# Kernel tuning notes

Measured on AMD Instinct MI355X. Metric: run time of the kernel, lower is better.

Reference implementation:

```python
import jax, jax.numpy as jnp
import numpy as np

WIDTH = 2048
NUM_HEADS = 16
HEAD_DIM = WIDTH // NUM_HEADS
BATCH = 16384


def block_diag_linear(x, w, b):
    # x: [..., width] -> [..., h, i] einsum with w: [h, i, j]
    xh = x.reshape(x.shape[:-1] + (NUM_HEADS, HEAD_DIM))
    y = jnp.einsum('...hi,hij->...hj', xh, w) + b
    return y.reshape(x.shape)


def setup_inputs() -> dict:
    key = jax.random.key(0)
    ks = jax.random.split(key, 7)
    x = jax.random.normal(ks[0], (BATCH, WIDTH), dtype=jnp.float32)
    state = jax.random.normal(ks[1], (BATCH, WIDTH), dtype=jnp.float32)
    w_in = jax.random.normal(ks[2], (NUM_HEADS, HEAD_DIM, HEAD_DIM), dtype=jnp.float32) * 0.02
    b_in = jax.random.normal(ks[3], (NUM_HEADS, HEAD_DIM), dtype=jnp.float32) * 0.02
    w_a = jax.random.normal(ks[4], (NUM_HEADS, HEAD_DIM, HEAD_DIM), dtype=jnp.float32) * 0.02
    b_a = jax.random.normal(ks[5], (NUM_HEADS, HEAD_DIM), dtype=jnp.float32) * 0.02
    a_param = jax.random.normal(ks[6], (WIDTH,), dtype=jnp.float32) * 0.5
    return {'x': x, 'state': state, 'w_in': w_in, 'b_in': b_in,
            'w_a': w_a, 'b_a': b_a, 'a_param': a_param}


def reference(x, state, w_in, b_in, w_a, b_a, a_param):
    gate_x = jax.nn.sigmoid(block_diag_linear(x, w_in, b_in))
    gate_a = jax.nn.sigmoid(block_diag_linear(x, w_a, b_a))
    log_a = -8.0 * gate_a * jax.nn.softplus(a_param)  # [B, width]
    a = jnp.exp(log_a)
    scale = jnp.sqrt(1.0 - jnp.exp(2.0 * log_a))
    return a * state + gate_x * x * scale
```

## Files before the change

### kernel.cpp

```cpp
#include <hip/hip_runtime.h>
#include <hip/hip_bf16.h>

typedef __attribute__((ext_vector_type(8))) short bf16x8;
typedef __attribute__((ext_vector_type(4))) float f32x4;
typedef __attribute__((ext_vector_type(4))) unsigned short u16x4;
typedef __attribute__((ext_vector_type(8))) unsigned short u16x8;

#define WIDTH  2048
#define NHEADS 16
#define HDIM   128
#define BM     64

__device__ __forceinline__ unsigned short f2bf(float f) {
  union { float f; unsigned int u; } v; v.f = f;
  unsigned int u = v.u;
  unsigned int r = (u + 0x7FFFu + ((u >> 16) & 1u)) >> 16;
  return (unsigned short)r;
}

__device__ __forceinline__ float bf2f(unsigned short s) {
  union { unsigned int u; float f; } v;
  v.u = ((unsigned int)s) << 16;
  return v.f;
}

__device__ __forceinline__ unsigned int pk_bf16(float lo, float hi) {
  __hip_bfloat162 b = __float22bfloat162_rn(make_float2(lo, hi));
  union { __hip_bfloat162 b; unsigned int u; } c; c.b = b;
  return c.u;
}

#define LOG2E 1.4426950408889634f

__global__ __launch_bounds__(256) void prep_kernel(
    const float* __restrict__ w_in, const float* __restrict__ w_a,
    const float* __restrict__ a_param,
    const float* __restrict__ b_in, const float* __restrict__ b_a,
    unsigned short* __restrict__ wTin, unsigned short* __restrict__ wTa,
    float* __restrict__ sp8, float* __restrict__ sbi, float* __restrict__ sba) {
  const int b = blockIdx.x;
  if (b >= 64) {
    int tid = (b - 64) * 256 + threadIdx.x;
    float v  = a_param[tid];
    float sp = (v > 20.0f) ? v : log1pf(__expf(v));
    sp8[tid] = 8.0f * sp * LOG2E;
    sbi[tid] = b_in[tid] * LOG2E;
    sba[tid] = b_a[tid] * LOG2E;
    return;
  }
  const int h  = b >> 2;
  const int i0 = (b & 3) * 32;
  __shared__ unsigned short tl[2][32][136];

  const float* s0 = w_in + h * 16384 + i0 * 128;
  const float* s1 = w_a  + h * 16384 + i0 * 128;
#pragma unroll
  for (int it = 0; it < 4; ++it) {
    int e = it * 1024 + threadIdx.x * 4;
    int r = e >> 7, c = e & 127;
    f32x4 v0 = *reinterpret_cast<const f32x4*>(s0 + r * 128 + c);
    f32x4 v1 = *reinterpret_cast<const f32x4*>(s1 + r * 128 + c);
#pragma unroll
    for (int k = 0; k < 4; ++k) {
      tl[0][r][c + k] = f2bf(v0[k] * LOG2E);
      tl[1][r][c + k] = f2bf(v1[k] * LOG2E);
    }
  }
  __syncthreads();

  const int j  = threadIdx.x >> 1;
  const int ih = (threadIdx.x & 1) * 16;
  u16x8 o0a, o0b, o1a, o1b;
#pragma unroll
  for (int k = 0; k < 8; ++k) {
    o0a[k] = tl[0][ih + k][j];      o0b[k] = tl[0][ih + 8 + k][j];
    o1a[k] = tl[1][ih + k][j];      o1b[k] = tl[1][ih + 8 + k][j];
  }
  unsigned short* d0 = wTin + h * 16384 + j * 128 + i0 + ih;
  unsigned short* d1 = wTa  + h * 16384 + j * 128 + i0 + ih;
  *reinterpret_cast<u16x8*>(d0)     = o0a;
  *reinterpret_cast<u16x8*>(d0 + 8) = o0b;
  *reinterpret_cast<u16x8*>(d1)     = o1a;
  *reinterpret_cast<u16x8*>(d1 + 8) = o1b;
}

__global__ __launch_bounds__(256, 4) void rglru_kernel(
    const float* __restrict__ x, const float* __restrict__ state,
    const float* __restrict__ sbi, const float* __restrict__ sba,
    const unsigned short* __restrict__ wTin, const unsigned short* __restrict__ wTa,
    const float* __restrict__ sp8, float* __restrict__ out) {
  __shared__ unsigned short xs[BM * HDIM];

  const int bid  = blockIdx.x;
  const int h    = bid & (NHEADS - 1);
  const int rb   = bid >> 4;
  const int t    = threadIdx.x;
  const int lane = t & 63;
  const int wid  = t >> 6;
  const int l15  = lane & 15;
  const int l4   = lane >> 4;

  const float* xtile = x + (long)rb * BM * WIDTH + h * HDIM;
#pragma unroll
  for (int it = 0; it < 8; ++it) {
    int idx = it * 256 + t;
    int r   = idx >> 5;
    int c4  = idx & 31;
    f32x4 v = __builtin_nontemporal_load(
        reinterpret_cast<const f32x4*>(xtile + (long)r * WIDTH) + c4);
    uint2 p;
    p.x = pk_bf16(v[0], v[1]);
    p.y = pk_bf16(v[2], v[3]);
    int off = (r * 256 + c4 * 8) ^ ((r & 7) << 4);
    *reinterpret_cast<uint2*>(reinterpret_cast<char*>(xs) + off) = p;
  }

  const int cb = h * HDIM + wid * 32 + l4 * 4;
  f32x4 bi0 = *reinterpret_cast<const f32x4*>(sbi + cb);
  f32x4 bi1 = *reinterpret_cast<const f32x4*>(sbi + cb + 16);
  f32x4 ba0 = *reinterpret_cast<const f32x4*>(sba + cb);
  f32x4 ba1 = *reinterpret_cast<const f32x4*>(sba + cb + 16);
  f32x4 sp0 = *reinterpret_cast<const f32x4*>(sp8 + cb);
  f32x4 sp1 = *reinterpret_cast<const f32x4*>(sp8 + cb + 16);

  __syncthreads();

  f32x4 acc_in[4][2], acc_a[4][2];
#pragma unroll
  for (int m = 0; m < 4; ++m) {
    acc_in[m][0] = bi0; acc_in[m][1] = bi1;
    acc_a[m][0]  = ba0; acc_a[m][1]  = ba1;
  }

  const unsigned short* wi0 = wTin + ((h * HDIM + wid * 32 + l15) * HDIM) + l4 * 8;
  const unsigned short* wi1 = wi0 + 16 * HDIM;
  const unsigned short* wa0 = wTa + ((h * HDIM + wid * 32 + l15) * HDIM) + l4 * 8;
  const unsigned short* wa1 = wa0 + 16 * HDIM;

  const int xsw = ((l15 & 7) << 4);

#pragma unroll
  for (int kk = 0; kk < 4; ++kk) {
    bf16x8 xfr[4];
#pragma unroll
    for (int m = 0; m < 4; ++m) {
      int boff = ((m * 16 + l15) * 256 + kk * 64 + l4 * 16) ^ xsw;
      xfr[m] = *reinterpret_cast<const bf16x8*>(
          reinterpret_cast<const char*>(xs) + boff);
    }
    bf16x8 win[2], wa[2];
    win[0] = *reinterpret_cast<const bf16x8*>(wi0 + kk * 32);
    win[1] = *reinterpret_cast<const bf16x8*>(wi1 + kk * 32);
    wa[0]  = *reinterpret_cast<const bf16x8*>(wa0 + kk * 32);
    wa[1]  = *reinterpret_cast<const bf16x8*>(wa1 + kk * 32);
#pragma unroll
    for (int m = 0; m < 4; ++m)
#pragma unroll
      for (int n = 0; n < 2; ++n) {
        acc_in[m][n] = __builtin_amdgcn_mfma_f32_16x16x32_bf16(
            win[n], xfr[m], acc_in[m][n], 0, 0, 0);
        acc_a[m][n] = __builtin_amdgcn_mfma_f32_16x16x32_bf16(
            wa[n], xfr[m], acc_a[m][n], 0, 0, 0);
      }
  }

  const long base = (long)(rb * BM + l15) * WIDTH + cb;
  const float* ps = state + base;
  float*       po = out + base;
  const char* pxs = reinterpret_cast<const char*>(xs);
  const int xe0 = (l15 * 256 + (wid * 32 + l4 * 4) * 2) ^ xsw;
  const int xe1 = (l15 * 256 + (wid * 32 + 16 + l4 * 4) * 2) ^ xsw;

#pragma unroll
  for (int m = 0; m < 4; ++m) {
#pragma unroll
    for (int n = 0; n < 2; ++n) {
      f32x4 sv = *reinterpret_cast<const f32x4*>(ps + n * 16);
      u16x4 xb = *reinterpret_cast<const u16x4*>(
          pxs + (n ? xe1 : xe0) + m * 4096);
      f32x4 sp = n ? sp1 : sp0;
      f32x4 o;
#pragma unroll
      for (int r = 0; r < 4; ++r) {
        float gx  = __builtin_amdgcn_rcpf(1.0f + exp2f(-acc_in[m][n][r]));
        float ga  = __builtin_amdgcn_rcpf(1.0f + exp2f(-acc_a[m][n][r]));
        float av  = exp2f(-ga * sp[r]);
        float sc  = sqrtf(fmaxf(1.0f - av * av, 0.0f));
        o[r] = av * sv[r] + gx * bf2f(xb[r]) * sc;
      }
      *reinterpret_cast<f32x4*>(po + n * 16) = o;
    }
    ps += 16 * WIDTH;
    po += 16 * WIDTH;
  }
}

extern "C" void kernel_launch(void* const* d_in, const int* in_sizes, int n_in,
                              void* d_out, int out_size, void* d_ws, size_t ws_size,
                              hipStream_t stream) {
  const float* x       = (const float*)d_in[0];
  const float* state   = (const float*)d_in[1];
  const float* w_in    = (const float*)d_in[2];
  const float* b_in    = (const float*)d_in[3];
  const float* w_a     = (const float*)d_in[4];
  const float* b_a     = (const float*)d_in[5];
  const float* a_param = (const float*)d_in[6];
  float* out = (float*)d_out;

  unsigned short* wTin = (unsigned short*)d_ws;
  unsigned short* wTa  = wTin + NHEADS * HDIM * HDIM;
  float*          sp8  = (float*)(wTa + NHEADS * HDIM * HDIM);
  float*          sbi  = sp8 + WIDTH;
  float*          sba  = sbi + WIDTH;

  hipLaunchKernelGGL(prep_kernel, dim3(72), dim3(256), 0, stream,
                     w_in, w_a, a_param, b_in, b_a, wTin, wTa, sp8, sbi, sba);

  hipLaunchKernelGGL(rglru_kernel, dim3(4096), dim3(256), 0, stream,
                     x, state, sbi, sba, wTin, wTa, sp8, out);
}
```

Baseline: 103.4 us.

## Drop shared-memory x staging; load x fragments directly and transpose via identity MFMA

Each wave now owns 16 rows and all 128 output columns of a head. It loads its x fragments straight from global memory into registers, which removes the LDS tile and the __syncthreads. In the epilogue, x values in the output layout come from an MFMA against an identity matrix instead of LDS reads. Each wave must now stream the full per-head weight matrix (8 column tiles) from global/L2, which raises weight load traffic and register pressure. The x loads are no longer nontemporal and read only 32-byte chunks per lane.

```diff
diff --git a/kernel.cpp b/kernel.cpp
--- a/kernel.cpp
+++ b/kernel.cpp
@@ -3,25 +3,17 @@
 
 typedef __attribute__((ext_vector_type(8))) short bf16x8;
 typedef __attribute__((ext_vector_type(4))) float f32x4;
-typedef __attribute__((ext_vector_type(4))) unsigned short u16x4;
 typedef __attribute__((ext_vector_type(8))) unsigned short u16x8;
 
 #define WIDTH  2048
 #define NHEADS 16
 #define HDIM   128
-#define BM     64
 
 __device__ __forceinline__ unsigned short f2bf(float f) {
   union { float f; unsigned int u; } v; v.f = f;
   unsigned int u = v.u;
   unsigned int r = (u + 0x7FFFu + ((u >> 16) & 1u)) >> 16;
   return (unsigned short)r;
-}
-
-__device__ __forceinline__ float bf2f(unsigned short s) {
-  union { unsigned int u; float f; } v;
-  v.u = ((unsigned int)s) << 16;
-  return v.f;
 }
 
 __device__ __forceinline__ unsigned int pk_bf16(float lo, float hi) {
@@ -89,8 +81,6 @@
     const float* __restrict__ sbi, const float* __restrict__ sba,
     const unsigned short* __restrict__ wTin, const unsigned short* __restrict__ wTa,
     const float* __restrict__ sp8, float* __restrict__ out) {
-  __shared__ unsigned short xs[BM * HDIM];
-
   const int bid  = blockIdx.x;
   const int h    = bid & (NHEADS - 1);
   const int rb   = bid >> 4;
@@ -100,98 +90,84 @@
   const int l15  = lane & 15;
   const int l4   = lane >> 4;
 
-  const float* xtile = x + (long)rb * BM * WIDTH + h * HDIM;
+  const int  r0   = rb * 64 + wid * 16;
+  const long rowo = (long)(r0 + l15) * WIDTH + h * HDIM;
+
+  const float* xrow = x + rowo + l4 * 8;
+  f32x4 xq[4][2];
 #pragma unroll
-  for (int it = 0; it < 8; ++it) {
-    int idx = it * 256 + t;
-    int r   = idx >> 5;
-    int c4  = idx & 31;
-    f32x4 v = __builtin_nontemporal_load(
-        reinterpret_cast<const f32x4*>(xtile + (long)r * WIDTH) + c4);
-    uint2 p;
-    p.x = pk_bf16(v[0], v[1]);
-    p.y = pk_bf16(v[2], v[3]);
-    int off = (r * 256 + c4 * 8) ^ ((r & 7) << 4);
-    *reinterpret_cast<uint2*>(reinterpret_cast<char*>(xs) + off) = p;
+  for (int kk = 0; kk < 4; ++kk) {
+    xq[kk][0] = *reinterpret_cast<const f32x4*>(xrow + kk * 32);
+    xq[kk][1] = *reinterpret_cast<const f32x4*>(xrow + kk * 32 + 4);
+  }
+  bf16x8 xfr[4];
+#pragma unroll
+  for (int kk = 0; kk < 4; ++kk) {
+    union { bf16x8 v; unsigned int u[4]; } uu;
+    uu.u[0] = pk_bf16(xq[kk][0][0], xq[kk][0][1]);
+    uu.u[1] = pk_bf16(xq[kk][0][2], xq[kk][0][3]);
+    uu.u[2] = pk_bf16(xq[kk][1][0], xq[kk][1][1]);
+    uu.u[3] = pk_bf16(xq[kk][1][2], xq[kk][1][3]);
+    xfr[kk] = uu.v;
   }
 
-  const int cb = h * HDIM + wid * 32 + l4 * 4;
-  f32x4 bi0 = *reinterpret_cast<const f32x4*>(sbi + cb);
-  f32x4 bi1 = *reinterpret_cast<const f32x4*>(sbi + cb + 16);
-  f32x4 ba0 = *reinterpret_cast<const f32x4*>(sba + cb);
-  f32x4 ba1 = *reinterpret_cast<const f32x4*>(sba + cb + 16);
-  f32x4 sp0 = *reinterpret_cast<const f32x4*>(sp8 + cb);
-  f32x4 sp1 = *reinterpret_cast<const f32x4*>(sp8 + cb + 16);
-
-  __syncthreads();
-
-  f32x4 acc_in[4][2], acc_a[4][2];
+  bf16x8 idf0, idf1;
+  {
+    union { bf16x8 v; unsigned short us[8]; } a0, a1;
 #pragma unroll
-  for (int m = 0; m < 4; ++m) {
-    acc_in[m][0] = bi0; acc_in[m][1] = bi1;
-    acc_a[m][0]  = ba0; acc_a[m][1]  = ba1;
+    for (int e = 0; e < 8; ++e) {
+      int k = l4 * 8 + e;
+      a0.us[e] = (k == l15)      ? (unsigned short)0x3F80 : (unsigned short)0;
+      a1.us[e] = (k == l15 + 16) ? (unsigned short)0x3F80 : (unsigned short)0;
+    }
+    idf0 = a0.v; idf1 = a1.v;
   }
 
-  const unsigned short* wi0 = wTin + ((h * HDIM + wid * 32 + l15) * HDIM) + l4 * 8;
-  const unsigned short* wi1 = wi0 + 16 * HDIM;
-  const unsigned short* wa0 = wTa + ((h * HDIM + wid * 32 + l15) * HDIM) + l4 * 8;
-  const unsigned short* wa1 = wa0 + 16 * HDIM;
+  const int cbase = h * HDIM + l4 * 4;
+  f32x4 acc_in[8], acc_a[8];
+#pragma unroll
+  for (int n = 0; n < 8; ++n) {
+    acc_in[n] = *reinterpret_cast<const f32x4*>(sbi + cbase + n * 16);
+    acc_a[n]  = *reinterpret_cast<const f32x4*>(sba + cbase + n * 16);
+  }
 
-  const int xsw = ((l15 & 7) << 4);
+  const unsigned short* wb0 = wTin + (h * HDIM + l15) * HDIM + l4 * 8;
+  const unsigned short* wb1 = wTa  + (h * HDIM + l15) * HDIM + l4 * 8;
 
 #pragma unroll
   for (int kk = 0; kk < 4; ++kk) {
-    bf16x8 xfr[4];
+    const unsigned short* w0 = wb0 + kk * 32;
+    const unsigned short* w1 = wb1 + kk * 32;
 #pragma unroll
-    for (int m = 0; m < 4; ++m) {
-      int boff = ((m * 16 + l15) * 256 + kk * 64 + l4 * 16) ^ xsw;
-      xfr[m] = *reinterpret_cast<const bf16x8*>(
-          reinterpret_cast<const char*>(xs) + boff);
+    for (int n = 0; n < 8; ++n) {
+      bf16x8 wi = *reinterpret_cast<const bf16x8*>(w0 + n * 16 * HDIM);
+      bf16x8 wv = *reinterpret_cast<const bf16x8*>(w1 + n * 16 * HDIM);
+      acc_in[n] = __builtin_amdgcn_mfma_f32_16x16x32_bf16(wi, xfr[kk], acc_in[n], 0, 0, 0);
+      acc_a[n]  = __builtin_amdgcn_mfma_f32_16x16x32_bf16(wv, xfr[kk], acc_a[n], 0, 0, 0);
     }
-    bf16x8 win[2], wa[2];
-    win[0] = *reinterpret_cast<const bf16x8*>(wi0 + kk * 32);
-    win[1] = *reinterpret_cast<const bf16x8*>(wi1 + kk * 32);
-    wa[0]  = *reinterpret_cast<const bf16x8*>(wa0 + kk * 32);
-    wa[1]  = *reinterpret_cast<const bf16x8*>(wa1 + kk * 32);
-#pragma unroll
-    for (int m = 0; m < 4; ++m)
-#pragma unroll
-      for (int n = 0; n < 2; ++n) {
-        acc_in[m][n] = __builtin_amdgcn_mfma_f32_16x16x32_bf16(
-            win[n], xfr[m], acc_in[m][n], 0, 0, 0);
-        acc_a[m][n] = __builtin_amdgcn_mfma_f32_16x16x32_bf16(
-            wa[n], xfr[m], acc_a[m][n], 0, 0, 0);
-      }
   }
 
-  const long base = (long)(rb * BM + l15) * WIDTH + cb;
-  const float* ps = state + base;
-  float*       po = out + base;
-  const char* pxs = reinterpret_cast<const char*>(xs);
-  const int xe0 = (l15 * 256 + (wid * 32 + l4 * 4) * 2) ^ xsw;
-  const int xe1 = (l15 * 256 + (wid * 32 + 16 + l4 * 4) * 2) ^ xsw;
+  const float* srow = state + rowo + l4 * 4;
+  float*       orow = out + rowo + l4 * 4;
+  const float* spb  = sp8 + cbase;
+  const f32x4  zero = (f32x4)(0.0f);
 
 #pragma unroll
-  for (int m = 0; m < 4; ++m) {
+  for (int n = 0; n < 8; ++n) {
+    f32x4 sv = *reinterpret_cast<const f32x4*>(srow + n * 16);
+    f32x4 sp = *reinterpret_cast<const f32x4*>(spb + n * 16);
+    f32x4 xt = __builtin_amdgcn_mfma_f32_16x16x32_bf16(
+        (n & 1) ? idf1 : idf0, xfr[n >> 1], zero, 0, 0, 0);
+    f32x4 o;
 #pragma unroll
-    for (int n = 0; n < 2; ++n) {
-      f32x4 sv = *reinterpret_cast<const f32x4*>(ps + n * 16);
-      u16x4 xb = *reinterpret_cast<const u16x4*>(
-          pxs + (n ? xe1 : xe0) + m * 4096);
-      f32x4 sp = n ? sp1 : sp0;
-      f32x4 o;
-#pragma unroll
-      for (int r = 0; r < 4; ++r) {
-        float gx  = __builtin_amdgcn_rcpf(1.0f + exp2f(-acc_in[m][n][r]));
-        float ga  = __builtin_amdgcn_rcpf(1.0f + exp2f(-acc_a[m][n][r]));
-        float av  = exp2f(-ga * sp[r]);
-        float sc  = sqrtf(fmaxf(1.0f - av * av, 0.0f));
-        o[r] = av * sv[r] + gx * bf2f(xb[r]) * sc;
-      }
-      *reinterpret_cast<f32x4*>(po + n * 16) = o;
+    for (int r = 0; r < 4; ++r) {
+      float gx = __builtin_amdgcn_rcpf(1.0f + exp2f(-acc_in[n][r]));
+      float ga = __builtin_amdgcn_rcpf(1.0f + exp2f(-acc_a[n][r]));
+      float av = exp2f(-ga * sp[r]);
+      float sc = sqrtf(fmaxf(1.0f - av * av, 0.0f));
+      o[r] = av * sv[r] + gx * xt[r] * sc;
     }
-    ps += 16 * WIDTH;
-    po += 16 * WIDTH;
+    *reinterpret_cast<f32x4*>(orow + n * 16) = o;
   }
 }
 
```

Result: slower. 224.2 us (+116.9%).

## Process two row tiles per block, prefetching second x tile during first compute

Applied to the files above, without the earlier changes.

Each block now handles two 64-row tiles instead of one, halving the grid. The second tile's x values are loaded into registers before the first tile's MFMA and epilogue run, then converted and written to a second LDS buffer. This overlaps global load latency with compute and amortises weight and bias loads across two tiles. In exchange it uses more registers and LDS per block, which may reduce occupancy, and leaves fewer blocks to balance across CUs.

```diff
diff --git a/kernel.cpp b/kernel.cpp
--- a/kernel.cpp
+++ b/kernel.cpp
@@ -89,30 +89,32 @@
     const float* __restrict__ sbi, const float* __restrict__ sba,
     const unsigned short* __restrict__ wTin, const unsigned short* __restrict__ wTa,
     const float* __restrict__ sp8, float* __restrict__ out) {
-  __shared__ unsigned short xs[BM * HDIM];
+  __shared__ unsigned short xs[2][BM * HDIM];
 
   const int bid  = blockIdx.x;
   const int h    = bid & (NHEADS - 1);
-  const int rb   = bid >> 4;
+  const int rbb  = bid >> 4;
   const int t    = threadIdx.x;
   const int lane = t & 63;
   const int wid  = t >> 6;
   const int l15  = lane & 15;
   const int l4   = lane >> 4;
 
-  const float* xtile = x + (long)rb * BM * WIDTH + h * HDIM;
+  const int r_  = t >> 5;
+  const int c4_ = t & 31;
+
+  const float* xt0 = x + (long)(rbb * 2 * BM) * WIDTH + h * HDIM;
+
 #pragma unroll
   for (int it = 0; it < 8; ++it) {
-    int idx = it * 256 + t;
-    int r   = idx >> 5;
-    int c4  = idx & 31;
+    int r = it * 8 + r_;
     f32x4 v = __builtin_nontemporal_load(
-        reinterpret_cast<const f32x4*>(xtile + (long)r * WIDTH) + c4);
+        reinterpret_cast<const f32x4*>(xt0 + (long)r * WIDTH) + c4_);
     uint2 p;
     p.x = pk_bf16(v[0], v[1]);
     p.y = pk_bf16(v[2], v[3]);
-    int off = (r * 256 + c4 * 8) ^ ((r & 7) << 4);
-    *reinterpret_cast<uint2*>(reinterpret_cast<char*>(xs) + off) = p;
+    int off = (r * 256 + c4_ * 8) ^ ((r & 7) << 4);
+    *reinterpret_cast<uint2*>(reinterpret_cast<char*>(xs[0]) + off) = p;
   }
 
   const int cb = h * HDIM + wid * 32 + l4 * 4;
@@ -123,75 +125,102 @@
   f32x4 sp0 = *reinterpret_cast<const f32x4*>(sp8 + cb);
   f32x4 sp1 = *reinterpret_cast<const f32x4*>(sp8 + cb + 16);
 
-  __syncthreads();
-
-  f32x4 acc_in[4][2], acc_a[4][2];
-#pragma unroll
-  for (int m = 0; m < 4; ++m) {
-    acc_in[m][0] = bi0; acc_in[m][1] = bi1;
-    acc_a[m][0]  = ba0; acc_a[m][1]  = ba1;
-  }
-
   const unsigned short* wi0 = wTin + ((h * HDIM + wid * 32 + l15) * HDIM) + l4 * 8;
   const unsigned short* wi1 = wi0 + 16 * HDIM;
   const unsigned short* wa0 = wTa + ((h * HDIM + wid * 32 + l15) * HDIM) + l4 * 8;
   const unsigned short* wa1 = wa0 + 16 * HDIM;
 
   const int xsw = ((l15 & 7) << 4);
-
-#pragma unroll
-  for (int kk = 0; kk < 4; ++kk) {
-    bf16x8 xfr[4];
-#pragma unroll
-    for (int m = 0; m < 4; ++m) {
-      int boff = ((m * 16 + l15) * 256 + kk * 64 + l4 * 16) ^ xsw;
-      xfr[m] = *reinterpret_cast<const bf16x8*>(
-          reinterpret_cast<const char*>(xs) + boff);
-    }
-    bf16x8 win[2], wa[2];
-    win[0] = *reinterpret_cast<const bf16x8*>(wi0 + kk * 32);
-    win[1] = *reinterpret_cast<const bf16x8*>(wi1 + kk * 32);
-    wa[0]  = *reinterpret_cast<const bf16x8*>(wa0 + kk * 32);
-    wa[1]  = *reinterpret_cast<const bf16x8*>(wa1 + kk * 32);
-#pragma unroll
-    for (int m = 0; m < 4; ++m)
-#pragma unroll
-      for (int n = 0; n < 2; ++n) {
-        acc_in[m][n] = __builtin_amdgcn_mfma_f32_16x16x32_bf16(
-            win[n], xfr[m], acc_in[m][n], 0, 0, 0);
-        acc_a[m][n] = __builtin_amdgcn_mfma_f32_16x16x32_bf16(
-            wa[n], xfr[m], acc_a[m][n], 0, 0, 0);
-      }
-  }
-
-  const long base = (long)(rb * BM + l15) * WIDTH + cb;
-  const float* ps = state + base;
-  float*       po = out + base;
-  const char* pxs = reinterpret_cast<const char*>(xs);
   const int xe0 = (l15 * 256 + (wid * 32 + l4 * 4) * 2) ^ xsw;
   const int xe1 = (l15 * 256 + (wid * 32 + 16 + l4 * 4) * 2) ^ xsw;
 
-#pragma unroll
-  for (int m = 0; m < 4; ++m) {
-#pragma unroll
-    for (int n = 0; n < 2; ++n) {
-      f32x4 sv = *reinterpret_cast<const f32x4*>(ps + n * 16);
-      u16x4 xb = *reinterpret_cast<const u16x4*>(
-          pxs + (n ? xe1 : xe0) + m * 4096);
-      f32x4 sp = n ? sp1 : sp0;
-      f32x4 o;
-#pragma unroll
-      for (int r = 0; r < 4; ++r) {
-        float gx  = __builtin_amdgcn_rcpf(1.0f + exp2f(-acc_in[m][n][r]));
-        float ga  = __builtin_amdgcn_rcpf(1.0f + exp2f(-acc_a[m][n][r]));
-        float av  = exp2f(-ga * sp[r]);
-        float sc  = sqrtf(fmaxf(1.0f - av * av, 0.0f));
-        o[r] = av * sv[r] + gx * bf2f(xb[r]) * sc;
+  __syncthreads();
+
+  f32x4 xa[8];
+  {
+    const float* xt1 = xt0 + (long)BM * WIDTH;
+#pragma unroll
+    for (int it = 0; it < 8; ++it) {
+      int r = it * 8 + r_;
+      xa[it] = __builtin_nontemporal_load(
+          reinterpret_cast<const f32x4*>(xt1 + (long)r * WIDTH) + c4_);
+    }
+  }
+
+#pragma unroll
+  for (int tile = 0; tile < 2; ++tile) {
+    f32x4 acc_in[4][2], acc_a[4][2];
+#pragma unroll
+    for (int m = 0; m < 4; ++m) {
+      acc_in[m][0] = bi0; acc_in[m][1] = bi1;
+      acc_a[m][0]  = ba0; acc_a[m][1]  = ba1;
+    }
+
+    const char* pxs = reinterpret_cast<const char*>(xs[tile]);
+
+#pragma unroll
+    for (int kk = 0; kk < 4; ++kk) {
+      bf16x8 xfr[4];
+#pragma unroll
+      for (int m = 0; m < 4; ++m) {
+        int boff = ((m * 16 + l15) * 256 + kk * 64 + l4 * 16) ^ xsw;
+        xfr[m] = *reinterpret_cast<const bf16x8*>(pxs + boff);
       }
-      *reinterpret_cast<f32x4*>(po + n * 16) = o;
-    }
-    ps += 16 * WIDTH;
-    po += 16 * WIDTH;
+      bf16x8 win[2], wa[2];
+      win[0] = *reinterpret_cast<const bf16x8*>(wi0 + kk * 32);
+      win[1] = *reinterpret_cast<const bf16x8*>(wi1 + kk * 32);
+      wa[0]  = *reinterpret_cast<const bf16x8*>(wa0 + kk * 32);
+      wa[1]  = *reinterpret_cast<const bf16x8*>(wa1 + kk * 32);
+#pragma unroll
+      for (int m = 0; m < 4; ++m)
+#pragma unroll
+        for (int n = 0; n < 2; ++n) {
+          acc_in[m][n] = __builtin_amdgcn_mfma_f32_16x16x32_bf16(
+              win[n], xfr[m], acc_in[m][n], 0, 0, 0);
+          acc_a[m][n] = __builtin_amdgcn_mfma_f32_16x16x32_bf16(
+              wa[n], xfr[m], acc_a[m][n], 0, 0, 0);
+        }
+    }
+
+    const long base = (long)(rbb * 2 * BM + tile * BM + l15) * WIDTH + cb;
+    const float* ps = state + base;
+    float*       po = out + base;
+
+#pragma unroll
+    for (int m = 0; m < 4; ++m) {
+#pragma unroll
+      for (int n = 0; n < 2; ++n) {
+        f32x4 sv = *reinterpret_cast<const f32x4*>(ps + n * 16);
+        u16x4 xb = *reinterpret_cast<const u16x4*>(
+            pxs + (n ? xe1 : xe0) + m * 4096);
+        f32x4 sp = n ? sp1 : sp0;
+        f32x4 o;
+#pragma unroll
+        for (int r = 0; r < 4; ++r) {
+          float gx  = __builtin_amdgcn_rcpf(1.0f + exp2f(-acc_in[m][n][r]));
+          float ga  = __builtin_amdgcn_rcpf(1.0f + exp2f(-acc_a[m][n][r]));
+          float av  = exp2f(-ga * sp[r]);
+          float sc  = sqrtf(fmaxf(1.0f - av * av, 0.0f));
+          o[r] = av * sv[r] + gx * bf2f(xb[r]) * sc;
+        }
+        *reinterpret_cast<f32x4*>(po + n * 16) = o;
+      }
+      ps += 16 * WIDTH;
+      po += 16 * WIDTH;
+    }
+
+    if (tile == 0) {
+#pragma unroll
+      for (int it = 0; it < 8; ++it) {
+        int r = it * 8 + r_;
+        uint2 p;
+        p.x = pk_bf16(xa[it][0], xa[it][1]);
+        p.y = pk_bf16(xa[it][2], xa[it][3]);
+        int off = (r * 256 + c4_ * 8) ^ ((r & 7) << 4);
+        *reinterpret_cast<uint2*>(reinterpret_cast<char*>(xs[1]) + off) = p;
+      }
+      __syncthreads();
+    }
   }
 }
 
@@ -216,6 +245,6 @@
   hipLaunchKernelGGL(prep_kernel, dim3(72), dim3(256), 0, stream,
                      w_in, w_a, a_param, b_in, b_a, wTin, wTa, sp8, sbi, sba);
 
-  hipLaunchKernelGGL(rglru_kernel, dim3(4096), dim3(256), 0, stream,
+  hipLaunchKernelGGL(rglru_kernel, dim3(2048), dim3(256), 0, stream,
                      x, state, sbi, sba, wTin, wTa, sp8, out);
 }
```

Measured after the change: 132.2 us. 27.9% more time.
